# Kernel tuning notes

Measured on AMD Instinct MI355X. Metric: run time of the kernel, lower is better.

Reference implementation:

```python
import jax, jax.numpy as jnp
import numpy as np

N_NODES = 100000; N_EDGES = 1600000; B = 16
IN_CH = 32; HID = 32; H1 = 4; OUT_CH = 32; H2 = 4; EDGE_DIM = 16
GMM_HID = 128; NUM_MIX = 3; ACTION_DIM = 10
NEG_SLOPE = 0.2  # PyG GATv2Conv default negative_slope


def _glorot(key, shape):
    return jax.random.normal(key, shape, dtype=jnp.float32) * (1.0 / np.sqrt(shape[-1]))


def setup_inputs() -> dict:
    key = jax.random.key(0)
    ks = jax.random.split(key, 20)
    x = jax.random.normal(ks[0], (N_NODES, IN_CH), jnp.float32)
    edge_index = jax.random.randint(ks[1], (2, N_EDGES), 0, N_NODES, dtype=jnp.int64)
    edge_attr = jax.random.normal(ks[2], (N_EDGES, EDGE_DIM), jnp.float32)
    batch = jnp.sort(jax.random.randint(ks[3], (N_NODES,), 0, B, dtype=jnp.int64))
    d1 = H1 * HID; d2 = H2 * OUT_CH
    return dict(
        x=x, edge_index=edge_index, edge_attr=edge_attr, batch=batch,
        W1l=_glorot(ks[4], (d1, IN_CH)), b1l=jnp.zeros((d1,), jnp.float32),
        W1r=_glorot(ks[5], (d1, IN_CH)), b1r=jnp.zeros((d1,), jnp.float32),
        W1e=_glorot(ks[6], (d1, EDGE_DIM)), att1=_glorot(ks[7], (H1, HID)),
        bias1=jnp.zeros((d1,), jnp.float32),
        W2l=_glorot(ks[8], (d2, d1)), b2l=jnp.zeros((d2,), jnp.float32),
        W2r=_glorot(ks[9], (d2, d1)), b2r=jnp.zeros((d2,), jnp.float32),
        W2e=_glorot(ks[10], (d2, EDGE_DIM)), att2=_glorot(ks[11], (H2, OUT_CH)),
        bias2=jnp.zeros((d2,), jnp.float32),
        Wg1=_glorot(ks[12], (GMM_HID, d2)), bg1=jnp.zeros((GMM_HID,), jnp.float32),
        Wg2=_glorot(ks[13], (NUM_MIX * 5, GMM_HID)), bg2=jnp.zeros((NUM_MIX * 5,), jnp.float32),
        Wp=_glorot(ks[14], (ACTION_DIM, d2)), bp=jnp.zeros((ACTION_DIM,), jnp.float32),
    )


def _gatv2(x, src, dst, ea, Wl, bl, Wr, br, We, att, bias, heads, ch):
    """PyG GATv2Conv with edge_dim, concat=True, add_self_loops=True (fill='mean'), eval mode."""
    N = x.shape[0]
    E = ea.shape[0]
    # self-loop edge_attr = mean of incoming edge attrs per target node (fill_value='mean')
    attr_sum = jax.ops.segment_sum(ea, dst, num_segments=N)
    cnt = jax.ops.segment_sum(jnp.ones((E, 1), ea.dtype), dst, num_segments=N)
    loop_attr = attr_sum / jnp.maximum(cnt, 1.0)
    loop = jnp.arange(N, dtype=src.dtype)
    s = jnp.concatenate([src, loop])
    d = jnp.concatenate([dst, loop])
    eaf = jnp.concatenate([ea, loop_attr], axis=0)  # [E+N, edge_dim]
    xl = (x @ Wl.T + bl).reshape(N, heads, ch)  # source transform (messages)
    xr = (x @ Wr.T + br).reshape(N, heads, ch)  # target transform
    ee = (eaf @ We.T).reshape(-1, heads, ch)
    m = jax.nn.leaky_relu(xl[s] + xr[d] + ee, NEG_SLOPE)  # [E+N, H, C]
    logit = jnp.einsum('ehc,hc->eh', m, att)  # attention logits per edge/head
    # segment softmax over edges sharing a target node (every node has a self-loop)
    mx = jax.ops.segment_max(logit, d, num_segments=N)
    ex = jnp.exp(logit - mx[d])
    den = jax.ops.segment_sum(ex, d, num_segments=N)
    alpha = ex / den[d]
    out = jax.ops.segment_sum(alpha[..., None] * xl[s], d, num_segments=N)  # [N, H, C]
    return out.reshape(N, heads * ch) + bias


def reference(x, edge_index, edge_attr, batch,
              W1l, b1l, W1r, b1r, W1e, att1, bias1,
              W2l, b2l, W2r, b2r, W2e, att2, bias2,
              Wg1, bg1, Wg2, bg2, Wp, bp):
    src, dst = edge_index[0], edge_index[1]
    y = jax.nn.elu(_gatv2(x, src, dst, edge_attr, W1l, b1l, W1r, b1r, W1e, att1, bias1, H1, HID))
    # dropout is identity in eval mode
    y = _gatv2(y, src, dst, edge_attr, W2l, b2l, W2r, b2r, W2e, att2, bias2, H2, OUT_CH)
    # global_mean_pool over batch
    gsum = jax.ops.segment_sum(y, batch, num_segments=B)
    gcnt = jax.ops.segment_sum(jnp.ones((y.shape[0], 1), y.dtype), batch, num_segments=B)
    g = gsum / jnp.maximum(gcnt, 1.0)  # [B, H2*OUT_CH]
    gmm_params = jax.nn.relu(g @ Wg1.T + bg1) @ Wg2.T + bg2  # [B, 15]
    num_proposals_logits = g @ Wp.T + bp  # [B, 10]
    return jnp.concatenate([gmm_params, num_proposals_logits], axis=-1)  # [B, 25]
```

## Files before the change

kernel.cpp:

```cpp
#include <hip/hip_runtime.h>
#include <math.h>

#define N_NODES 100000
#define N_EDGES 1600000
#define EN_TOT  (N_EDGES + N_NODES)
#define BATCH   16
#define EDGE_DIM 16
#define NEG_SLOPE 0.2f
#define NB_SCAN 391
#define LOG2E 1.44269504f

typedef float v2f __attribute__((ext_vector_type(2)));

__device__ __forceinline__ int rfl(int v) { return __builtin_amdgcn_readfirstlane(v); }

__device__ __forceinline__ v2f fma2(v2f a, v2f b, v2f c) {
#if __has_builtin(__builtin_elementwise_fma)
    return __builtin_elementwise_fma(a, b, c);
#else
    v2f r; r.x = fmaf(a.x, b.x, c.x); r.y = fmaf(a.y, b.y, c.y); return r;
#endif
}

__device__ __forceinline__ float red16(float p) {
    p += __int_as_float(__builtin_amdgcn_ds_swizzle(__float_as_int(p), 0x041F));
    p += __int_as_float(__builtin_amdgcn_ds_swizzle(__float_as_int(p), 0x081F));
    p += __int_as_float(__builtin_amdgcn_ds_swizzle(__float_as_int(p), 0x101F));
    p += __int_as_float(__builtin_amdgcn_ds_swizzle(__float_as_int(p), 0x201F));
    return p;
}

__global__ void zero_kernel(float* __restrict__ p, long long n) {
    long long i = (long long)blockIdx.x * blockDim.x + threadIdx.x;
    long long stride = (long long)gridDim.x * blockDim.x;
    for (; i < n; i += stride) p[i] = 0.0f;
}

__global__ void count_deg(const int* __restrict__ dst, int* __restrict__ deg) {
    int e = blockIdx.x * 256 + threadIdx.x;
    if (e < N_EDGES) atomicAdd(&deg[dst[e]], 1);
}

__global__ __launch_bounds__(256) void scan1(const int* __restrict__ deg,
                                             int* __restrict__ incl, int* __restrict__ bsum) {
    __shared__ int s[256];
    int n = blockIdx.x * 256 + threadIdx.x;
    int v = (n < N_NODES) ? deg[n] + 1 : 0;
    s[threadIdx.x] = v;
    __syncthreads();
    for (int off = 1; off < 256; off <<= 1) {
        int t = (threadIdx.x >= off) ? s[threadIdx.x - off] : 0;
        __syncthreads();
        s[threadIdx.x] += t;
        __syncthreads();
    }
    if (n < N_NODES) incl[n] = s[threadIdx.x];
    if (threadIdx.x == 255) bsum[blockIdx.x] = s[255];
}

__global__ __launch_bounds__(512) void scan2(int* __restrict__ bsum) {
    __shared__ int s[512];
    int t = threadIdx.x;
    int v = (t < NB_SCAN) ? bsum[t] : 0;
    s[t] = v;
    __syncthreads();
    for (int off = 1; off < 512; off <<= 1) {
        int u = (t >= off) ? s[t - off] : 0;
        __syncthreads();
        s[t] += u;
        __syncthreads();
    }
    if (t < NB_SCAN) bsum[t] = s[t] - v;
}

__global__ void scan3(const int* __restrict__ incl, const int* __restrict__ deg,
                      const int* __restrict__ bsum, int* __restrict__ offs) {
    int n = blockIdx.x * 256 + threadIdx.x;
    if (n < N_NODES) offs[n] = incl[n] - (deg[n] + 1) + bsum[blockIdx.x];
    if (n == 0) offs[N_NODES] = EN_TOT;
}

__global__ void scatter(const int* __restrict__ src, const int* __restrict__ dst,
                        const int* __restrict__ offs, int* __restrict__ cursor,
                        int2* __restrict__ csr) {
    int e = blockIdx.x * 256 + threadIdx.x;
    if (e < N_EDGES) {
        int d = dst[e];
        int r = atomicAdd(&cursor[d], 1);
        csr[offs[d] + r] = make_int2(src[e], e);
    } else if (e < EN_TOT) {
        int n = e - N_EDGES;
        csr[offs[n + 1] - 1] = make_int2(n, N_EDGES + n);
    }
}

__global__ __launch_bounds__(256) void loopattr_csr(const int* __restrict__ offs,
                                                    const int2* __restrict__ csr,
                                                    const float* __restrict__ ea,
                                                    float* __restrict__ lattr) {
    int node = blockIdx.x * 4 + (threadIdx.x >> 6);
    if (node >= N_NODES) return;
    int lane = threadIdx.x & 63;
    int row = offs[node];
    int degn = offs[node + 1] - 1 - row;
    int k = lane & 15, grp = lane >> 4;
    float acc = 0.0f;
    for (int i = grp; i < degn; i += 4) {
        int eid = csr[row + i].y;
        acc += ea[(long long)eid * EDGE_DIM + k];
    }
    acc += __shfl_xor(acc, 16);
    acc += __shfl_xor(acc, 32);
    if (lane < 16) lattr[(long long)node * EDGE_DIM + k] = acc / fmaxf((float)degn, 1.0f);
}

template<int K>
__global__ __launch_bounds__(256) void dual_linear(
    const float* __restrict__ in,
    const float* __restrict__ Wl, const float* __restrict__ bl,
    const float* __restrict__ Wr, const float* __restrict__ br,
    float* __restrict__ outl, float* __restrict__ outr, int N)
{
    constexpr int ROWS = 32;
    constexpr int K2 = K / 2;
    __shared__ float2 srow[ROWS][K2];
    int t = threadIdx.x;
    int base = blockIdx.x * ROWS;
    {
        const float2* in2 = (const float2*)in;
        for (int i = t; i < ROWS * K2; i += 256) {
            int r = i / K2, k = i - r * K2;
            int n = base + r;
            srow[r][k] = (n < N) ? in2[(size_t)n * K2 + k] : make_float2(0.f, 0.f);
        }
    }
    __syncthreads();
    const float* W  = (t < 128) ? Wl : Wr;
    const float* bb = (t < 128) ? bl : br;
    float* outp     = (t < 128) ? outl : outr;
    int j = t & 127;
    float bj = bb[j];
    float acc[ROWS];
#pragma unroll
    for (int r = 0; r < ROWS; ++r) acc[r] = bj;
    const float2* W2 = (const float2*)(W + (size_t)j * K);
    for (int kk = 0; kk < K2; ++kk) {
        float2 w = W2[kk];
#pragma unroll
        for (int r = 0; r < ROWS; ++r) {
            float2 a = srow[r][kk];
            acc[r] = fmaf(a.x, w.x, acc[r]);
            acc[r] = fmaf(a.y, w.y, acc[r]);
        }
    }
    for (int r = 0; r < ROWS; ++r) {
        int n = base + r;
        if (n < N) outp[(long long)n * 128 + j] = acc[r];
    }
}

template<int DO_ELU>
__global__ __launch_bounds__(256) void gat_fused(
    const int* __restrict__ offs, const int2* __restrict__ csr,
    const float* __restrict__ ea, const float* __restrict__ lattr,
    const float* __restrict__ We, const float* __restrict__ att,
    const v2f* __restrict__ xl2, const v2f* __restrict__ xr2,
    const float* __restrict__ bias, float* __restrict__ y)
{
    int node = blockIdx.x * 4 + (threadIdx.x >> 6);
    if (node >= N_NODES) return;
    int lane = threadIdx.x & 63;
    int c = lane << 1;

    v2f we0[8], we1[8];
    {
        const v2f* Wa = (const v2f*)(We + (size_t)c * EDGE_DIM);
        const v2f* Wb = (const v2f*)(We + (size_t)(c + 1) * EDGE_DIM);
#pragma unroll
        for (int q = 0; q < 8; ++q) { we0[q] = Wa[q]; we1[q] = Wb[q]; }
    }
    float2 atv = ((const float2*)att)[lane];
    float att0 = atv.x * LOG2E, att1 = atv.y * LOG2E;
    const float THR = 8.0f * LOG2E;

    int row  = rfl(offs[node]);
    int rend = rfl(offs[node + 1]);
    int last = rend - 1;
    v2f xrv = xr2[(size_t)node * 64 + lane];

    float m = -INFINITY, d = 0.f, acc0 = 0.f, acc1 = 0.f;

    auto attr_ptr = [&](int eid) -> const float4* {
        return (const float4*)((eid < N_EDGES) ? ea + (size_t)eid * EDGE_DIM
                                               : lattr + (size_t)(eid - N_EDGES) * EDGE_DIM);
    };

    auto body = [&](float4 A0, float4 A1, float4 A2, float4 A3, v2f xls) {
        v2f a[8] = { {A0.x,A0.y},{A0.z,A0.w},{A1.x,A1.y},{A1.z,A1.w},
                     {A2.x,A2.y},{A2.z,A2.w},{A3.x,A3.y},{A3.z,A3.w} };
        v2f ee0 = {0.f,0.f}, ee1 = {0.f,0.f};
#pragma unroll
        for (int q = 0; q < 8; ++q) {
            ee0 = fma2(a[q], we0[q], ee0);
            ee1 = fma2(a[q], we1[q], ee1);
        }
        float v0 = xls.x + xrv.x + ee0.x + ee0.y;
        float v1 = xls.y + xrv.y + ee1.x + ee1.y;
        v0 = fmaxf(v0, NEG_SLOPE * v0);
        v1 = fmaxf(v1, NEG_SLOPE * v1);
        float pl = red16(fmaf(v0, att0, v1 * att1));
        if (pl - m > THR) { float r_ = exp2f(m - pl); d *= r_; acc0 *= r_; acc1 *= r_; m = pl; }
        float w = exp2f(pl - m);
        d += w;
        acc0 = fmaf(w, xls.x, acc0);
        acc1 = fmaf(w, xls.y, acc1);
    };

    int2 seA = csr[row];
    const float4* apA = attr_ptr(seA.y);
    float4 Aa0 = apA[0], Aa1 = apA[1], Aa2 = apA[2], Aa3 = apA[3];
    v2f xlA = xl2[(size_t)seA.x * 64 + lane];

    int jB = min(row + 1, last);
    int2 seB = csr[jB];
    const float4* apB = attr_ptr(seB.y);
    float4 Ab0 = apB[0], Ab1 = apB[1], Ab2 = apB[2], Ab3 = apB[3];
    v2f xlB = xl2[(size_t)seB.x * 64 + lane];

    int i = row;
    for (; i + 1 < rend; i += 2) {
        body(Aa0, Aa1, Aa2, Aa3, xlA);
        {
            int j = min(i + 2, last);
            seA = csr[j];
            const float4* ap = attr_ptr(seA.y);
            Aa0 = ap[0]; Aa1 = ap[1]; Aa2 = ap[2]; Aa3 = ap[3];
            xlA = xl2[(size_t)seA.x * 64 + lane];
        }
        body(Ab0, Ab1, Ab2, Ab3, xlB);
        {
            int j = min(i + 3, last);
            seB = csr[j];
            const float4* ap = attr_ptr(seB.y);
            Ab0 = ap[0]; Ab1 = ap[1]; Ab2 = ap[2]; Ab3 = ap[3];
            xlB = xl2[(size_t)seB.x * 64 + lane];
        }
    }
    if (i < rend) body(Aa0, Aa1, Aa2, Aa3, xlA);

    float2 bv = ((const float2*)bias)[lane];
    float o0 = acc0 / d + bv.x;
    float o1 = acc1 / d + bv.y;
    if (DO_ELU) {
        o0 = (o0 > 0.0f) ? o0 : (__expf(o0) - 1.0f);
        o1 = (o1 > 0.0f) ? o1 : (__expf(o1) - 1.0f);
    }
    *(float2*)(y + (size_t)node * 128 + c) = make_float2(o0, o1);
}

__global__ __launch_bounds__(256) void pool_csr(const float* __restrict__ y,
                                                const int* __restrict__ batch,
                                                float* __restrict__ gsum,
                                                float* __restrict__ gcnt) {
    int base = blockIdx.x * 256;
    int t = threadIdx.x;
    int c = t & 127, h = t >> 7;
    int n = base + h;
    int end = min(base + 256, N_NODES);
    if (n >= end) return;
    float acc = 0.0f, cnt = 0.0f;
    int curb = batch[n];
    for (; n < end; n += 2) {
        int b = batch[n];
        if (b != curb) {
            atomicAdd(&gsum[curb * 128 + c], acc);
            if (c == 0) atomicAdd(&gcnt[curb], cnt);
            acc = 0.0f; cnt = 0.0f; curb = b;
        }
        acc += y[(long long)n * 128 + c];
        cnt += 1.0f;
    }
    atomicAdd(&gsum[curb * 128 + c], acc);
    if (c == 0) atomicAdd(&gcnt[curb], cnt);
}

__global__ __launch_bounds__(128) void head_kernel(
    const float* __restrict__ gsum, const float* __restrict__ gcnt,
    const float* __restrict__ Wg1, const float* __restrict__ bg1,
    const float* __restrict__ Wg2, const float* __restrict__ bg2,
    const float* __restrict__ Wp, const float* __restrict__ bp,
    float* __restrict__ out)
{
    int b = blockIdx.x;
    int j = threadIdx.x;
    __shared__ float g[128], h[128];
    float cntv = fmaxf(gcnt[b], 1.0f);
    g[j] = gsum[b * 128 + j] / cntv;
    __syncthreads();
    float a = bg1[j];
    for (int k = 0; k < 128; ++k) a += g[k] * Wg1[j * 128 + k];
    h[j] = fmaxf(a, 0.0f);
    __syncthreads();
    if (j < 15) {
        float o = bg2[j];
        for (int k = 0; k < 128; ++k) o += h[k] * Wg2[j * 128 + k];
        out[b * 25 + j] = o;
    }
    if (j >= 64 && j < 74) {
        int p = j - 64;
        float o = bp[p];
        for (int k = 0; k < 128; ++k) o += g[k] * Wp[p * 128 + k];
        out[b * 25 + 15 + p] = o;
    }
}

extern "C" void kernel_launch(void* const* d_in, const int* in_sizes, int n_in,
                              void* d_out, int out_size, void* d_ws, size_t ws_size,
                              hipStream_t stream)
{
    const float* x     = (const float*)d_in[0];
    const int*   ei    = (const int*)  d_in[1];
    const float* ea    = (const float*)d_in[2];
    const int*   batch = (const int*)  d_in[3];
    const float* W1l = (const float*)d_in[4],  *b1l  = (const float*)d_in[5];
    const float* W1r = (const float*)d_in[6],  *b1r  = (const float*)d_in[7];
    const float* W1e = (const float*)d_in[8],  *att1 = (const float*)d_in[9];
    const float* bias1 = (const float*)d_in[10];
    const float* W2l = (const float*)d_in[11], *b2l  = (const float*)d_in[12];
    const float* W2r = (const float*)d_in[13], *b2r  = (const float*)d_in[14];
    const float* W2e = (const float*)d_in[15], *att2 = (const float*)d_in[16];
    const float* bias2 = (const float*)d_in[17];
    const float* Wg1 = (const float*)d_in[18], *bg1 = (const float*)d_in[19];
    const float* Wg2 = (const float*)d_in[20], *bg2 = (const float*)d_in[21];
    const float* Wp  = (const float*)d_in[22], *bp  = (const float*)d_in[23];
    const int* src = ei;
    const int* dst = ei + N_EDGES;

    float* ws = (float*)d_ws;
    size_t o = 0;
    float* xl    = ws + o; o += (size_t)N_NODES * 128;
    float* xr    = ws + o; o += (size_t)N_NODES * 128;
    float* y     = ws + o; o += (size_t)N_NODES * 128;
    float* lattr = ws + o; o += (size_t)N_NODES * EDGE_DIM;
    int2* csr    = (int2*)(ws + o); o += (size_t)EN_TOT * 2;
    int* offs    = (int*)(ws + o); o += (size_t)N_NODES + 2;
    int* deg     = (int*)(ws + o); o += (size_t)N_NODES;
    int* cursor  = (int*)(ws + o); o += (size_t)N_NODES;
    float* gsum  = ws + o; o += (size_t)BATCH * 128;
    float* gcnt  = ws + o; o += (size_t)BATCH;
    int* bsum    = (int*)(ws + o); o += 512;
    int* incl    = (int*)y;

    float* out = (float*)d_out;

    long long nz = (long long)N_NODES * 2 + BATCH * 128 + BATCH;
    zero_kernel<<<512, 256, 0, stream>>>((float*)deg, nz);

    count_deg<<<(N_EDGES + 255) / 256, 256, 0, stream>>>(dst, deg);
    scan1<<<NB_SCAN, 256, 0, stream>>>(deg, incl, bsum);
    scan2<<<1, 512, 0, stream>>>(bsum);
    scan3<<<NB_SCAN, 256, 0, stream>>>(incl, deg, bsum, offs);
    scatter<<<(EN_TOT + 255) / 256, 256, 0, stream>>>(src, dst, offs, cursor, csr);
    loopattr_csr<<<(N_NODES + 3) / 4, 256, 0, stream>>>(offs, csr, ea, lattr);

    const int GAT_BLK = (N_NODES + 3) / 4;

    dual_linear<32><<<(N_NODES + 31) / 32, 256, 0, stream>>>(x, W1l, b1l, W1r, b1r, xl, xr, N_NODES);
    gat_fused<1><<<GAT_BLK, 256, 0, stream>>>(offs, csr, ea, lattr,
                                              W1e, att1, (const v2f*)xl, (const v2f*)xr, bias1, y);

    dual_linear<128><<<(N_NODES + 31) / 32, 256, 0, stream>>>(y, W2l, b2l, W2r, b2r, xl, xr, N_NODES);
    gat_fused<0><<<GAT_BLK, 256, 0, stream>>>(offs, csr, ea, lattr,
                                              W2e, att2, (const v2f*)xl, (const v2f*)xr, bias2, y);

    pool_csr<<<(N_NODES + 255) / 256, 256, 0, stream>>>(y, batch, gsum, gcnt);
    head_kernel<<<BATCH, 128, 0, stream>>>(gsum, gcnt, Wg1, bg1, Wg2, bg2, Wp, bp, out);
}
```

Measured before the change: 929.4 us.

## Retile dual_linear to 64 rows with 2x2 output register blocking

The dual linear kernel now handles 64 rows per block. Each thread computes two output columns for both the left and right projections over 16 rows, instead of one column of one projection over all rows. Each shared-memory row load now feeds four weight vectors, which raises register-level reuse, and outputs are written as float2. Each thread now issues more scattered weight loads, and the larger tile doubles shared memory use for K=128, which may lower occupancy.

```diff
diff --git a/kernel.cpp b/kernel.cpp
--- a/kernel.cpp
+++ b/kernel.cpp
@@ -121,7 +121,7 @@
     const float* __restrict__ Wr, const float* __restrict__ br,
     float* __restrict__ outl, float* __restrict__ outr, int N)
 {
-    constexpr int ROWS = 32;
+    constexpr int ROWS = 64;
     constexpr int K2 = K / 2;
     __shared__ float2 srow[ROWS][K2];
     int t = threadIdx.x;
@@ -135,27 +135,34 @@
         }
     }
     __syncthreads();
-    const float* W  = (t < 128) ? Wl : Wr;
-    const float* bb = (t < 128) ? bl : br;
-    float* outp     = (t < 128) ? outl : outr;
-    int j = t & 127;
-    float bj = bb[j];
-    float acc[ROWS];
+    int q = t & 63;
+    int rbase = (t >> 6) * 16;
+    int c0 = q << 1, c1 = c0 + 1;
+    float al0[16], al1[16], ar0[16], ar1[16];
+    float bl0 = bl[c0], bl1 = bl[c1], br0 = br[c0], br1 = br[c1];
 #pragma unroll
-    for (int r = 0; r < ROWS; ++r) acc[r] = bj;
-    const float2* W2 = (const float2*)(W + (size_t)j * K);
+    for (int r = 0; r < 16; ++r) { al0[r] = bl0; al1[r] = bl1; ar0[r] = br0; ar1[r] = br1; }
+    const float2* Wl0 = (const float2*)(Wl + (size_t)c0 * K);
+    const float2* Wl1 = (const float2*)(Wl + (size_t)c1 * K);
+    const float2* Wr0 = (const float2*)(Wr + (size_t)c0 * K);
+    const float2* Wr1 = (const float2*)(Wr + (size_t)c1 * K);
     for (int kk = 0; kk < K2; ++kk) {
-        float2 w = W2[kk];
+        float2 w0 = Wl0[kk], w1 = Wl1[kk], w2 = Wr0[kk], w3 = Wr1[kk];
 #pragma unroll
-        for (int r = 0; r < ROWS; ++r) {
-            float2 a = srow[r][kk];
-            acc[r] = fmaf(a.x, w.x, acc[r]);
-            acc[r] = fmaf(a.y, w.y, acc[r]);
-        }
-    }
-    for (int r = 0; r < ROWS; ++r) {
-        int n = base + r;
-        if (n < N) outp[(long long)n * 128 + j] = acc[r];
+        for (int r = 0; r < 16; ++r) {
+            float2 a = srow[rbase + r][kk];
+            al0[r] = fmaf(a.x, w0.x, al0[r]); al0[r] = fmaf(a.y, w0.y, al0[r]);
+            al1[r] = fmaf(a.x, w1.x, al1[r]); al1[r] = fmaf(a.y, w1.y, al1[r]);
+            ar0[r] = fmaf(a.x, w2.x, ar0[r]); ar0[r] = fmaf(a.y, w2.y, ar0[r]);
+            ar1[r] = fmaf(a.x, w3.x, ar1[r]); ar1[r] = fmaf(a.y, w3.y, ar1[r]);
+        }
+    }
+    for (int r = 0; r < 16; ++r) {
+        int n = base + rbase + r;
+        if (n < N) {
+            *(float2*)(outl + (size_t)n * 128 + c0) = make_float2(al0[r], al1[r]);
+            *(float2*)(outr + (size_t)n * 128 + c0) = make_float2(ar0[r], ar1[r]);
+        }
     }
 }
 
@@ -364,12 +371,13 @@
     loopattr_csr<<<(N_NODES + 3) / 4, 256, 0, stream>>>(offs, csr, ea, lattr);
 
     const int GAT_BLK = (N_NODES + 3) / 4;
-
-    dual_linear<32><<<(N_NODES + 31) / 32, 256, 0, stream>>>(x, W1l, b1l, W1r, b1r, xl, xr, N_NODES);
+    const int DL_BLK  = (N_NODES + 63) / 64;
+
+    dual_linear<32><<<DL_BLK, 256, 0, stream>>>(x, W1l, b1l, W1r, b1r, xl, xr, N_NODES);
     gat_fused<1><<<GAT_BLK, 256, 0, stream>>>(offs, csr, ea, lattr,
                                               W1e, att1, (const v2f*)xl, (const v2f*)xr, bias1, y);
 
-    dual_linear<128><<<(N_NODES + 31) / 32, 256, 0, stream>>>(y, W2l, b2l, W2r, b2r, xl, xr, N_NODES);
+    dual_linear<128><<<DL_BLK, 256, 0, stream>>>(y, W2l, b2l, W2r, b2r, xl, xr, N_NODES);
     gat_fused<0><<<GAT_BLK, 256, 0, stream>>>(offs, csr, ea, lattr,
                                               W2e, att2, (const v2f*)xl, (const v2f*)xr, bias2, y);
 
```

New measurement: 1.061 ms. 1.14x slower.
